# Performance work log

Measured on AMD Instinct MI355X. Metric: run time of the kernel, lower is better.

## Reference

```python
import jax, jax.numpy as jnp
import numpy as np

B, TQ, TY = 8, 400, 400
Q_DIM, Y_DIM, ATT_DIM = 256, 256, 128


def setup_inputs() -> dict:
    key = jax.random.key(0)
    ks = jax.random.split(key, 9)
    s_q = 1.0 / np.sqrt(Q_DIM)
    s_y = 1.0 / np.sqrt(Y_DIM)
    s_a = 1.0 / np.sqrt(ATT_DIM)
    return {
        "query": jax.random.normal(ks[0], (B, TQ, Q_DIM), jnp.float32),
        "y": jax.random.normal(ks[1], (B, TY, Y_DIM), jnp.float32),
        "Wq_w": jax.random.uniform(ks[2], (ATT_DIM, Q_DIM), jnp.float32, -s_q, s_q),
        "Wq_b": jax.random.uniform(ks[3], (ATT_DIM,), jnp.float32, -s_q, s_q),
        "Wy_w": jax.random.uniform(ks[4], (ATT_DIM, Y_DIM), jnp.float32, -s_y, s_y),
        "Wy_b": jax.random.uniform(ks[5], (ATT_DIM,), jnp.float32, -s_y, s_y),
        "v_w": jax.random.uniform(ks[6], (1, ATT_DIM), jnp.float32, -s_a, s_a),
        "v_b": jax.random.uniform(ks[7], (1,), jnp.float32, -s_a, s_a),
        "n_wins_y": jax.random.randint(ks[8], (B,), TY // 2, TY + 1, jnp.int64 if jax.config.jax_enable_x64 else jnp.int32),
    }


def reference(query, y, Wq_w, Wq_b, Wy_w, Wy_b, v_w, v_b, n_wins_y):
    # Bahdanau scores: tanh(Wq(q)[:,None,:,:] + Wy(y)[:,:,None,:]) -> [B,Ty,Tq,A]
    q_proj = jnp.einsum('bqd,ad->bqa', query, Wq_w) + Wq_b      # [B,Tq,A]
    y_proj = jnp.einsum('btd,ad->bta', y, Wy_w) + Wy_b          # [B,Ty,A]
    h = jnp.tanh(q_proj[:, None, :, :] + y_proj[:, :, None, :])  # [B,Ty,Tq,A]
    att = jnp.einsum('btqa,a->btq', h, v_w[0]) + v_b[0]          # [B,Ty,Tq]
    att = jnp.transpose(att, (0, 2, 1))                          # [B,Tq,Ty]
    # mask invalid y windows (dim 2 = Ty), then softmax over Ty
    mask = jnp.arange(att.shape[2])[None, None, :] < n_wins_y[:, None, None]
    att = jnp.where(mask, att, -jnp.inf)
    att = jax.nn.softmax(att, axis=2)
    # soft attention apply: bmm(att, y) -> [B,Tq,y_dim]
    return jnp.einsum('bqt,btd->bqd', att, y)
```

## Files before the change

kernel.cpp:

```cpp
#include <hip/hip_runtime.h>


#define LOG2E 1.4426950408889634f
#define TANH_SCALE 2.8853900817779268f

constexpr int TQn = 400, TYn = 400, AD = 128, DD = 256;
constexpr int QT = 8;
constexpr int QBLOCKS = TQn / QT;
constexpr int YT = 64;
constexpr int NTT = 7;
constexpr int SSTR = 65;
constexpr int AQT = 8;
constexpr int AT3 = 16;
constexpr int PSTR = 449;

__global__ __launch_bounds__(128, 4) void proj_kernel(
    const float* __restrict__ qin, const float* __restrict__ yin,
    const float* __restrict__ Wq, const float* __restrict__ bq,
    const float* __restrict__ Wy, const float* __restrict__ by,
    float* __restrict__ Eq, float* __restrict__ Ey)
{
    const int blk = blockIdx.x;
    const bool is_q = blk < 800;
    const int row0 = (is_q ? blk : blk - 800) * 4;
    const float* in   = (is_q ? qin : yin) + (size_t)row0 * DD;
    const float* W    = is_q ? Wq : Wy;
    const float* bias = is_q ? bq : by;
    float* outp = (is_q ? Eq : Ey) + (size_t)row0 * AD;

    __shared__ float lin[4 * DD];
    {
        const float4* in4 = reinterpret_cast<const float4*>(in);
        float4* l4s = reinterpret_cast<float4*>(lin);
        l4s[threadIdx.x]       = in4[threadIdx.x];
        l4s[threadIdx.x + 128] = in4[threadIdx.x + 128];
    }
    __syncthreads();

    const int a = threadIdx.x;
    float acc0 = 0.f, acc1 = 0.f, acc2 = 0.f, acc3 = 0.f;
    const float4* w4p = reinterpret_cast<const float4*>(W + (size_t)a * DD);
    const float4* l4  = reinterpret_cast<const float4*>(lin);
    #pragma unroll 8
    for (int d4 = 0; d4 < 64; ++d4) {
        float4 w4 = w4p[d4];
        float4 v0 = l4[d4], v1 = l4[64 + d4], v2 = l4[128 + d4], v3 = l4[192 + d4];
        acc0 = fmaf(w4.x, v0.x, acc0); acc0 = fmaf(w4.y, v0.y, acc0);
        acc0 = fmaf(w4.z, v0.z, acc0); acc0 = fmaf(w4.w, v0.w, acc0);
        acc1 = fmaf(w4.x, v1.x, acc1); acc1 = fmaf(w4.y, v1.y, acc1);
        acc1 = fmaf(w4.z, v1.z, acc1); acc1 = fmaf(w4.w, v1.w, acc1);
        acc2 = fmaf(w4.x, v2.x, acc2); acc2 = fmaf(w4.y, v2.y, acc2);
        acc2 = fmaf(w4.z, v2.z, acc2); acc2 = fmaf(w4.w, v2.w, acc2);
        acc3 = fmaf(w4.x, v3.x, acc3); acc3 = fmaf(w4.y, v3.y, acc3);
        acc3 = fmaf(w4.z, v3.z, acc3); acc3 = fmaf(w4.w, v3.w, acc3);
    }
    const float bb = bias[a];
    outp[(size_t)0 * AD + a] = __builtin_amdgcn_exp2f((acc0 + bb) * TANH_SCALE);
    outp[(size_t)1 * AD + a] = __builtin_amdgcn_exp2f((acc1 + bb) * TANH_SCALE);
    outp[(size_t)2 * AD + a] = __builtin_amdgcn_exp2f((acc2 + bb) * TANH_SCALE);
    outp[(size_t)3 * AD + a] = __builtin_amdgcn_exp2f((acc3 + bb) * TANH_SCALE);
}

__global__ __launch_bounds__(512, 2) void score_kernel(
    const float* __restrict__ Eq,
    const float* __restrict__ Ey,
    const float* __restrict__ vw,
    const int*  __restrict__ nwins,
    float* __restrict__ s)
{
    const int bid = blockIdx.x;
    const int b   = bid / (QBLOCKS * NTT);
    const int rem = bid % (QBLOCKS * NTT);
    const int qt  = rem / NTT;
    const int tt  = rem % NTT;
    const int n   = nwins[b];
    const int t0  = tt * YT;
    if (t0 >= n) return;
    const int q0 = qt * QT;

    __shared__ float4 s_eq[QT * 32];
    __shared__ float4 s_v4[32];
    __shared__ float4 s_ey[32 * SSTR];

    const int tid  = threadIdx.x;
    const int wave = tid >> 6;
    const int lane = tid & 63;
    const int pcol = tid & 31;
    const int prow = tid >> 5;

    {
        const float4* eyb = reinterpret_cast<const float4*>(Ey);
        const size_t base = (size_t)(b * TYn) * 32 + pcol;
        const int r1 = min(t0 + prow + 16, TYn - 1);
        const int r2 = min(t0 + prow + 32, TYn - 1);
        const int r3 = min(t0 + prow + 48, TYn - 1);
        s_ey[pcol * SSTR + prow     ] = eyb[base + (size_t)(t0 + prow) * 32];
        s_ey[pcol * SSTR + prow + 16] = eyb[base + (size_t)r1 * 32];
        s_ey[pcol * SSTR + prow + 32] = eyb[base + (size_t)r2 * 32];
        s_ey[pcol * SSTR + prow + 48] = eyb[base + (size_t)r3 * 32];
    }
    if (tid < QT * 32) {
        s_eq[tid] = reinterpret_cast<const float4*>(Eq + (size_t)(b * TQn + q0) * AD)[tid];
    } else if (tid < QT * 32 + 32) {
        float4 v = reinterpret_cast<const float4*>(vw)[tid - QT * 32];
        s_v4[tid - QT * 32] = make_float4(-2.f * v.x, -2.f * v.y, -2.f * v.z, -2.f * v.w);
    }
    __syncthreads();

    float ac0 = 0.f, ac1 = 0.f, ac2 = 0.f, ac3 = 0.f;
    const float4* qrow = s_eq + wave * 32;
    #pragma unroll 8
    for (int a4 = 0; a4 < 32; ++a4) {
        float4 yv = s_ey[a4 * SSTR + lane];
        float4 qv = qrow[a4];
        float4 vv = s_v4[a4];
        float a0 = fmaf(qv.x, yv.x, 1.f);
        float a1 = fmaf(qv.y, yv.y, 1.f);
        float a2 = fmaf(qv.z, yv.z, 1.f);
        float a3 = fmaf(qv.w, yv.w, 1.f);
        float p01 = a0 * a1, p23 = a2 * a3;
        float R = __builtin_amdgcn_rcpf(p01 * p23);
        float u = p23 * R, v = p01 * R;
        ac0 = fmaf(vv.x, a1 * u, ac0);
        ac1 = fmaf(vv.y, a0 * u, ac1);
        ac2 = fmaf(vv.z, a3 * v, ac2);
        ac3 = fmaf(vv.w, a2 * v, ac3);
    }
    const int t = t0 + lane;
    if (t < TYn)
        s[(size_t)(b * TQn + q0 + wave) * TYn + t] = (ac0 + ac1) + (ac2 + ac3);
}

__global__ __launch_bounds__(512, 2) void apply_kernel(
    const float* __restrict__ y,
    const float* __restrict__ s,
    const int*  __restrict__ nwins,
    float* __restrict__ out)
{
    const int bid = blockIdx.x;
    const int b   = bid / QBLOCKS;
    const int q0  = (bid % QBLOCKS) * AQT;
    const int tid = threadIdx.x, wave = tid >> 6, lane = tid & 63;
    const int n = nwins[b];
    const float NEG_INF = -__builtin_inff();

    __shared__ float  s_p[AQT][PSTR];
    __shared__ float4 s_y[2][AT3 * 64];

    const float* srow = s + (size_t)(b * TQn + q0 + wave) * TYn;
    float sc0, sc1, sc2, sc3, sc4, sc5, sc6;
    {
        int t;
        t = 0 * 64 + lane; sc0 = (t < n) ? srow[t] : NEG_INF;
        t = 1 * 64 + lane; sc1 = (t < n) ? srow[t] : NEG_INF;
        t = 2 * 64 + lane; sc2 = (t < n) ? srow[t] : NEG_INF;
        t = 3 * 64 + lane; sc3 = (t < n) ? srow[t] : NEG_INF;
        t = 4 * 64 + lane; sc4 = (t < n) ? srow[t] : NEG_INF;
        t = 5 * 64 + lane; sc5 = (t < n) ? srow[t] : NEG_INF;
        t = 6 * 64 + lane; sc6 = (t < n) ? srow[t] : NEG_INF;
    }
    float m = fmaxf(fmaxf(fmaxf(sc0, sc1), fmaxf(sc2, sc3)),
                    fmaxf(fmaxf(sc4, sc5), sc6));
    #pragma unroll
    for (int off = 32; off >= 1; off >>= 1) m = fmaxf(m, __shfl_xor(m, off, 64));
    sc0 = __builtin_amdgcn_exp2f((sc0 - m) * LOG2E);
    sc1 = __builtin_amdgcn_exp2f((sc1 - m) * LOG2E);
    sc2 = __builtin_amdgcn_exp2f((sc2 - m) * LOG2E);
    sc3 = __builtin_amdgcn_exp2f((sc3 - m) * LOG2E);
    sc4 = __builtin_amdgcn_exp2f((sc4 - m) * LOG2E);
    sc5 = __builtin_amdgcn_exp2f((sc5 - m) * LOG2E);
    sc6 = __builtin_amdgcn_exp2f((sc6 - m) * LOG2E);
    float l = ((sc0 + sc1) + (sc2 + sc3)) + ((sc4 + sc5) + sc6);
    #pragma unroll
    for (int off = 32; off >= 1; off >>= 1) l += __shfl_xor(l, off, 64);
    const float inv = 1.0f / l;
    s_p[wave][0 * 64 + lane] = sc0 * inv;
    s_p[wave][1 * 64 + lane] = sc1 * inv;
    s_p[wave][2 * 64 + lane] = sc2 * inv;
    s_p[wave][3 * 64 + lane] = sc3 * inv;
    s_p[wave][4 * 64 + lane] = sc4 * inv;
    s_p[wave][5 * 64 + lane] = sc5 * inv;
    s_p[wave][6 * 64 + lane] = sc6 * inv;

    const float4* yb = reinterpret_cast<const float4*>(y) + (size_t)(b * TYn) * 64;
    const int scol = tid & 63, srow0 = tid >> 6;
    float4 g0 = yb[(size_t)(srow0    ) * 64 + scol];
    float4 g1 = yb[(size_t)(srow0 + 8) * 64 + scol];

    const int qa = ((wave & 3) << 1) + (lane >> 5);
    const int d4 = ((wave >> 2) << 5) + (lane & 31);
    float4 acc = {0.f, 0.f, 0.f, 0.f};
    const int ntile = (n + AT3 - 1) / AT3;

    __syncthreads();
    for (int i = 0; i < ntile; ++i) {
        float4* buf = s_y[i & 1];
        buf[srow0 * 64 + scol]       = g0;
        buf[(srow0 + 8) * 64 + scol] = g1;
        if (i + 1 < ntile) {
            const int t0n = (i + 1) * AT3;
            g0 = yb[(size_t)(t0n + srow0    ) * 64 + scol];
            g1 = yb[(size_t)(t0n + srow0 + 8) * 64 + scol];
        }
        __syncthreads();
        const int tb = i * AT3;
        #pragma unroll
        for (int ttl = 0; ttl < AT3; ++ttl) {
            float  pt = s_p[qa][tb + ttl];
            float4 yv = buf[ttl * 64 + d4];
            acc.x = fmaf(pt, yv.x, acc.x);
            acc.y = fmaf(pt, yv.y, acc.y);
            acc.z = fmaf(pt, yv.z, acc.z);
            acc.w = fmaf(pt, yv.w, acc.w);
        }
    }
    reinterpret_cast<float4*>(out)[(size_t)(b * TQn + q0 + qa) * 64 + d4] = acc;
}

extern "C" void kernel_launch(void* const* d_in, const int* in_sizes, int n_in,
                              void* d_out, int out_size, void* d_ws, size_t ws_size,
                              hipStream_t stream) {
    const float* query = (const float*)d_in[0];
    const float* y     = (const float*)d_in[1];
    const float* Wq_w  = (const float*)d_in[2];
    const float* Wq_b  = (const float*)d_in[3];
    const float* Wy_w  = (const float*)d_in[4];
    const float* Wy_b  = (const float*)d_in[5];
    const float* v_w   = (const float*)d_in[6];
    const int* nw      = (const int*)d_in[8];
    float* out = (float*)d_out;

    float* Eq = (float*)d_ws;
    float* Ey = Eq + (size_t)8 * TQn * AD;
    float* s  = Ey + (size_t)8 * TYn * AD;

    proj_kernel<<<1600, 128, 0, stream>>>(query, y, Wq_w, Wq_b, Wy_w, Wy_b, Eq, Ey);
    score_kernel<<<8 * QBLOCKS * NTT, 512, 0, stream>>>(Eq, Ey, v_w, nw, s);
    apply_kernel<<<8 * QBLOCKS, 512, 0, stream>>>(y, s, nw, out);
}
```

Measured before the change: 75.30 us.

## Transpose weights, split-K projection, and retile score/apply kernels for 256 threads

Adds a weight transpose kernel so projection loads of W are coalesced across threads, and reworks the projection into 8-row blocks with a two-way split over the reduction dimension plus a shared-memory reduction. The score kernel now computes 4 queries per thread over a quarter of the attention dim and reduces with cross-lane shuffles, which reuses each Ey load across queries. The apply kernel moves to 4 queries per 256-thread block and issues its y prefetch before the softmax. These changes aim at uncoalesced weight reads and low register-level reuse, at the cost of an extra kernel launch and more shuffle and reduction overhead.

```diff
diff --git a/kernel.cpp b/kernel.cpp
--- a/kernel.cpp
+++ b/kernel.cpp
@@ -5,63 +5,76 @@
 #define TANH_SCALE 2.8853900817779268f
 
 constexpr int TQn = 400, TYn = 400, AD = 128, DD = 256;
-constexpr int QT = 8;
-constexpr int QBLOCKS = TQn / QT;
-constexpr int YT = 64;
-constexpr int NTT = 7;
 constexpr int SSTR = 65;
-constexpr int AQT = 8;
-constexpr int AT3 = 16;
-constexpr int PSTR = 449;
-
-__global__ __launch_bounds__(128, 4) void proj_kernel(
+
+__global__ __launch_bounds__(128) void transpose_kernel(
+    const float* __restrict__ Wq, const float* __restrict__ Wy,
+    float4* __restrict__ WTq, float4* __restrict__ WTy)
+{
+    const int k4 = blockIdx.x & 63;
+    const bool isq = blockIdx.x < 64;
+    const float4* src = reinterpret_cast<const float4*>(isq ? Wq : Wy);
+    float4* dst = isq ? WTq : WTy;
+    const int a = threadIdx.x;
+    dst[k4 * 128 + a] = src[a * 64 + k4];
+}
+
+__global__ __launch_bounds__(256, 4) void proj_kernel(
     const float* __restrict__ qin, const float* __restrict__ yin,
-    const float* __restrict__ Wq, const float* __restrict__ bq,
-    const float* __restrict__ Wy, const float* __restrict__ by,
+    const float4* __restrict__ WTq, const float* __restrict__ bq,
+    const float4* __restrict__ WTy, const float* __restrict__ by,
     float* __restrict__ Eq, float* __restrict__ Ey)
 {
     const int blk = blockIdx.x;
-    const bool is_q = blk < 800;
-    const int row0 = (is_q ? blk : blk - 800) * 4;
+    const bool is_q = blk < 400;
+    const int row0 = (is_q ? blk : blk - 400) * 8;
     const float* in   = (is_q ? qin : yin) + (size_t)row0 * DD;
-    const float* W    = is_q ? Wq : Wy;
+    const float4* wt  = is_q ? WTq : WTy;
     const float* bias = is_q ? bq : by;
     float* outp = (is_q ? Eq : Ey) + (size_t)row0 * AD;
 
-    __shared__ float lin[4 * DD];
+    __shared__ float lin[8 * DD];
+    __shared__ float red[8][AD];
     {
         const float4* in4 = reinterpret_cast<const float4*>(in);
         float4* l4s = reinterpret_cast<float4*>(lin);
         l4s[threadIdx.x]       = in4[threadIdx.x];
-        l4s[threadIdx.x + 128] = in4[threadIdx.x + 128];
-    }
-    __syncthreads();
-
-    const int a = threadIdx.x;
-    float acc0 = 0.f, acc1 = 0.f, acc2 = 0.f, acc3 = 0.f;
-    const float4* w4p = reinterpret_cast<const float4*>(W + (size_t)a * DD);
-    const float4* l4  = reinterpret_cast<const float4*>(lin);
+        l4s[threadIdx.x + 256] = in4[threadIdx.x + 256];
+    }
+    __syncthreads();
+
+    const int a = threadIdx.x & 127;
+    const int h = threadIdx.x >> 7;
+    float acc[8] = {0.f,0.f,0.f,0.f,0.f,0.f,0.f,0.f};
+    const float4* l4 = reinterpret_cast<const float4*>(lin);
     #pragma unroll 8
-    for (int d4 = 0; d4 < 64; ++d4) {
-        float4 w4 = w4p[d4];
-        float4 v0 = l4[d4], v1 = l4[64 + d4], v2 = l4[128 + d4], v3 = l4[192 + d4];
-        acc0 = fmaf(w4.x, v0.x, acc0); acc0 = fmaf(w4.y, v0.y, acc0);
-        acc0 = fmaf(w4.z, v0.z, acc0); acc0 = fmaf(w4.w, v0.w, acc0);
-        acc1 = fmaf(w4.x, v1.x, acc1); acc1 = fmaf(w4.y, v1.y, acc1);
-        acc1 = fmaf(w4.z, v1.z, acc1); acc1 = fmaf(w4.w, v1.w, acc1);
-        acc2 = fmaf(w4.x, v2.x, acc2); acc2 = fmaf(w4.y, v2.y, acc2);
-        acc2 = fmaf(w4.z, v2.z, acc2); acc2 = fmaf(w4.w, v2.w, acc2);
-        acc3 = fmaf(w4.x, v3.x, acc3); acc3 = fmaf(w4.y, v3.y, acc3);
-        acc3 = fmaf(w4.z, v3.z, acc3); acc3 = fmaf(w4.w, v3.w, acc3);
-    }
-    const float bb = bias[a];
-    outp[(size_t)0 * AD + a] = __builtin_amdgcn_exp2f((acc0 + bb) * TANH_SCALE);
-    outp[(size_t)1 * AD + a] = __builtin_amdgcn_exp2f((acc1 + bb) * TANH_SCALE);
-    outp[(size_t)2 * AD + a] = __builtin_amdgcn_exp2f((acc2 + bb) * TANH_SCALE);
-    outp[(size_t)3 * AD + a] = __builtin_amdgcn_exp2f((acc3 + bb) * TANH_SCALE);
-}
-
-__global__ __launch_bounds__(512, 2) void score_kernel(
+    for (int i = 0; i < 32; ++i) {
+        const int k4 = h * 32 + i;
+        float4 w4 = wt[k4 * 128 + a];
+        #pragma unroll
+        for (int r = 0; r < 8; ++r) {
+            float4 v = l4[r * 64 + k4];
+            acc[r] = fmaf(w4.x, v.x, acc[r]);
+            acc[r] = fmaf(w4.y, v.y, acc[r]);
+            acc[r] = fmaf(w4.z, v.z, acc[r]);
+            acc[r] = fmaf(w4.w, v.w, acc[r]);
+        }
+    }
+    if (h) {
+        #pragma unroll
+        for (int r = 0; r < 8; ++r) red[r][a] = acc[r];
+    }
+    __syncthreads();
+    if (!h) {
+        const float bb = bias[a];
+        #pragma unroll
+        for (int r = 0; r < 8; ++r)
+            outp[(size_t)r * AD + a] =
+                __builtin_amdgcn_exp2f((acc[r] + red[r][a] + bb) * TANH_SCALE);
+    }
+}
+
+__global__ __launch_bounds__(256, 4) void score_kernel(
     const float* __restrict__ Eq,
     const float* __restrict__ Ey,
     const float* __restrict__ vw,
@@ -69,83 +82,103 @@
     float* __restrict__ s)
 {
     const int bid = blockIdx.x;
-    const int b   = bid / (QBLOCKS * NTT);
-    const int rem = bid % (QBLOCKS * NTT);
-    const int qt  = rem / NTT;
-    const int tt  = rem % NTT;
+    const int b   = bid / 700;
+    const int rem = bid % 700;
+    const int qg  = rem / 7;
+    const int tt  = rem % 7;
     const int n   = nwins[b];
-    const int t0  = tt * YT;
+    const int t0  = tt * 64;
     if (t0 >= n) return;
-    const int q0 = qt * QT;
-
-    __shared__ float4 s_eq[QT * 32];
+    const int q0 = qg * 4;
+
+    __shared__ float4 s_ey[32 * SSTR];
+    __shared__ float4 s_eq4[4 * 32];
     __shared__ float4 s_v4[32];
-    __shared__ float4 s_ey[32 * SSTR];
 
     const int tid  = threadIdx.x;
-    const int wave = tid >> 6;
-    const int lane = tid & 63;
     const int pcol = tid & 31;
     const int prow = tid >> 5;
-
     {
         const float4* eyb = reinterpret_cast<const float4*>(Ey);
         const size_t base = (size_t)(b * TYn) * 32 + pcol;
-        const int r1 = min(t0 + prow + 16, TYn - 1);
-        const int r2 = min(t0 + prow + 32, TYn - 1);
-        const int r3 = min(t0 + prow + 48, TYn - 1);
-        s_ey[pcol * SSTR + prow     ] = eyb[base + (size_t)(t0 + prow) * 32];
-        s_ey[pcol * SSTR + prow + 16] = eyb[base + (size_t)r1 * 32];
-        s_ey[pcol * SSTR + prow + 32] = eyb[base + (size_t)r2 * 32];
-        s_ey[pcol * SSTR + prow + 48] = eyb[base + (size_t)r3 * 32];
-    }
-    if (tid < QT * 32) {
-        s_eq[tid] = reinterpret_cast<const float4*>(Eq + (size_t)(b * TQn + q0) * AD)[tid];
-    } else if (tid < QT * 32 + 32) {
-        float4 v = reinterpret_cast<const float4*>(vw)[tid - QT * 32];
-        s_v4[tid - QT * 32] = make_float4(-2.f * v.x, -2.f * v.y, -2.f * v.z, -2.f * v.w);
-    }
-    __syncthreads();
-
+        #pragma unroll
+        for (int k = 0; k < 8; ++k) {
+            const int rt = min(t0 + prow + 8 * k, TYn - 1);
+            s_ey[pcol * SSTR + prow + 8 * k] = eyb[base + (size_t)rt * 32];
+        }
+    }
+    if (tid < 128) {
+        s_eq4[tid] = reinterpret_cast<const float4*>(Eq + (size_t)(b * TQn + q0) * AD)[tid];
+    } else if (tid < 160) {
+        float4 v = reinterpret_cast<const float4*>(vw)[tid - 128];
+        s_v4[tid - 128] = make_float4(-2.f * v.x, -2.f * v.y, -2.f * v.z, -2.f * v.w);
+    }
+    __syncthreads();
+
+    const int lane = tid & 63;
+    const int wave = tid >> 6;
+    const int tloc = (wave << 4) | (lane & 15);
+    const int ag   = lane >> 4;
     float ac0 = 0.f, ac1 = 0.f, ac2 = 0.f, ac3 = 0.f;
-    const float4* qrow = s_eq + wave * 32;
-    #pragma unroll 8
-    for (int a4 = 0; a4 < 32; ++a4) {
-        float4 yv = s_ey[a4 * SSTR + lane];
-        float4 qv = qrow[a4];
-        float4 vv = s_v4[a4];
-        float a0 = fmaf(qv.x, yv.x, 1.f);
-        float a1 = fmaf(qv.y, yv.y, 1.f);
-        float a2 = fmaf(qv.z, yv.z, 1.f);
-        float a3 = fmaf(qv.w, yv.w, 1.f);
-        float p01 = a0 * a1, p23 = a2 * a3;
-        float R = __builtin_amdgcn_rcpf(p01 * p23);
-        float u = p23 * R, v = p01 * R;
-        ac0 = fmaf(vv.x, a1 * u, ac0);
-        ac1 = fmaf(vv.y, a0 * u, ac1);
-        ac2 = fmaf(vv.z, a3 * v, ac2);
-        ac3 = fmaf(vv.w, a2 * v, ac3);
-    }
-    const int t = t0 + lane;
-    if (t < TYn)
-        s[(size_t)(b * TQn + q0 + wave) * TYn + t] = (ac0 + ac1) + (ac2 + ac3);
-}
-
-__global__ __launch_bounds__(512, 2) void apply_kernel(
+    #pragma unroll
+    for (int i = 0; i < 8; ++i) {
+        const int a4 = ag * 8 + i;
+        const float4 yv = s_ey[a4 * SSTR + tloc];
+        const float4 vv = s_v4[a4];
+        #define SCORE_Q(ACC, QQ)                                            \
+        {                                                                   \
+            float4 qv = s_eq4[(QQ) * 32 + a4];                              \
+            float a0 = fmaf(qv.x, yv.x, 1.f);                               \
+            float a1 = fmaf(qv.y, yv.y, 1.f);                               \
+            float a2 = fmaf(qv.z, yv.z, 1.f);                               \
+            float a3 = fmaf(qv.w, yv.w, 1.f);                               \
+            float p01 = a0 * a1, p23 = a2 * a3;                             \
+            float R = __builtin_amdgcn_rcpf(p01 * p23);                     \
+            float u = p23 * R, w = p01 * R;                                 \
+            ACC = fmaf(vv.x, a1 * u, ACC);                                  \
+            ACC = fmaf(vv.y, a0 * u, ACC);                                  \
+            ACC = fmaf(vv.z, a3 * w, ACC);                                  \
+            ACC = fmaf(vv.w, a2 * w, ACC);                                  \
+        }
+        SCORE_Q(ac0, 0) SCORE_Q(ac1, 1) SCORE_Q(ac2, 2) SCORE_Q(ac3, 3)
+        #undef SCORE_Q
+    }
+    ac0 += __shfl_xor(ac0, 16, 64); ac0 += __shfl_xor(ac0, 32, 64);
+    ac1 += __shfl_xor(ac1, 16, 64); ac1 += __shfl_xor(ac1, 32, 64);
+    ac2 += __shfl_xor(ac2, 16, 64); ac2 += __shfl_xor(ac2, 32, 64);
+    ac3 += __shfl_xor(ac3, 16, 64); ac3 += __shfl_xor(ac3, 32, 64);
+    const int t = t0 + tloc;
+    if (ag == 0 && t < TYn) {
+        const size_t o = (size_t)(b * TQn + q0) * TYn + t;
+        s[o]            = ac0;
+        s[o + TYn]      = ac1;
+        s[o + 2 * TYn]  = ac2;
+        s[o + 3 * TYn]  = ac3;
+    }
+}
+
+__global__ __launch_bounds__(256, 4) void apply_kernel(
     const float* __restrict__ y,
     const float* __restrict__ s,
     const int*  __restrict__ nwins,
     float* __restrict__ out)
 {
     const int bid = blockIdx.x;
-    const int b   = bid / QBLOCKS;
-    const int q0  = (bid % QBLOCKS) * AQT;
+    const int b   = bid / 100;
+    const int q0  = (bid % 100) * 4;
     const int tid = threadIdx.x, wave = tid >> 6, lane = tid & 63;
     const int n = nwins[b];
     const float NEG_INF = -__builtin_inff();
 
-    __shared__ float  s_p[AQT][PSTR];
-    __shared__ float4 s_y[2][AT3 * 64];
+    __shared__ float  s_p[4][408];
+    __shared__ float4 s_y[2][16 * 64];
+
+    const float4* yb = reinterpret_cast<const float4*>(y) + (size_t)(b * TYn) * 64;
+    const int scol = tid & 63, srow0 = tid >> 6;
+    float4 g0 = yb[(size_t)(srow0     ) * 64 + scol];
+    float4 g1 = yb[(size_t)(srow0 +  4) * 64 + scol];
+    float4 g2 = yb[(size_t)(srow0 +  8) * 64 + scol];
+    float4 g3 = yb[(size_t)(srow0 + 12) * 64 + scol];
 
     const float* srow = s + (size_t)(b * TQn + q0 + wave) * TYn;
     float sc0, sc1, sc2, sc3, sc4, sc5, sc6;
@@ -180,41 +213,43 @@
     s_p[wave][3 * 64 + lane] = sc3 * inv;
     s_p[wave][4 * 64 + lane] = sc4 * inv;
     s_p[wave][5 * 64 + lane] = sc5 * inv;
-    s_p[wave][6 * 64 + lane] = sc6 * inv;
-
-    const float4* yb = reinterpret_cast<const float4*>(y) + (size_t)(b * TYn) * 64;
-    const int scol = tid & 63, srow0 = tid >> 6;
-    float4 g0 = yb[(size_t)(srow0    ) * 64 + scol];
-    float4 g1 = yb[(size_t)(srow0 + 8) * 64 + scol];
-
-    const int qa = ((wave & 3) << 1) + (lane >> 5);
-    const int d4 = ((wave >> 2) << 5) + (lane & 31);
+    {
+        const int t = 6 * 64 + lane;
+        if (t < TYn) s_p[wave][t] = sc6 * inv;
+    }
+
+    const int q  = lane >> 4;
+    const int d4 = (wave << 4) | (lane & 15);
     float4 acc = {0.f, 0.f, 0.f, 0.f};
-    const int ntile = (n + AT3 - 1) / AT3;
+    const int ntile = (n + 15) >> 4;
 
     __syncthreads();
     for (int i = 0; i < ntile; ++i) {
         float4* buf = s_y[i & 1];
-        buf[srow0 * 64 + scol]       = g0;
-        buf[(srow0 + 8) * 64 + scol] = g1;
+        buf[(srow0     ) * 64 + scol] = g0;
+        buf[(srow0 +  4) * 64 + scol] = g1;
+        buf[(srow0 +  8) * 64 + scol] = g2;
+        buf[(srow0 + 12) * 64 + scol] = g3;
         if (i + 1 < ntile) {
-            const int t0n = (i + 1) * AT3;
-            g0 = yb[(size_t)(t0n + srow0    ) * 64 + scol];
-            g1 = yb[(size_t)(t0n + srow0 + 8) * 64 + scol];
+            const int t0n = (i + 1) * 16;
+            g0 = yb[(size_t)(t0n + srow0     ) * 64 + scol];
+            g1 = yb[(size_t)(t0n + srow0 +  4) * 64 + scol];
+            g2 = yb[(size_t)(t0n + srow0 +  8) * 64 + scol];
+            g3 = yb[(size_t)(t0n + srow0 + 12) * 64 + scol];
         }
         __syncthreads();
-        const int tb = i * AT3;
-        #pragma unroll
-        for (int ttl = 0; ttl < AT3; ++ttl) {
-            float  pt = s_p[qa][tb + ttl];
-            float4 yv = buf[ttl * 64 + d4];
+        const int tb = i * 16;
+        #pragma unroll
+        for (int ttl = 0; ttl < 16; ++ttl) {
+            const float  pt = s_p[q][tb + ttl];
+            const float4 yv = buf[ttl * 64 + d4];
             acc.x = fmaf(pt, yv.x, acc.x);
             acc.y = fmaf(pt, yv.y, acc.y);
             acc.z = fmaf(pt, yv.z, acc.z);
             acc.w = fmaf(pt, yv.w, acc.w);
         }
     }
-    reinterpret_cast<float4*>(out)[(size_t)(b * TQn + q0 + qa) * 64 + d4] = acc;
+    reinterpret_cast<float4*>(out)[(size_t)(b * TQn + q0 + q) * 64 + d4] = acc;
 }
 
 extern "C" void kernel_launch(void* const* d_in, const int* in_sizes, int n_in,
@@ -230,11 +265,14 @@
     const int* nw      = (const int*)d_in[8];
     float* out = (float*)d_out;
 
-    float* Eq = (float*)d_ws;
-    float* Ey = Eq + (size_t)8 * TQn * AD;
-    float* s  = Ey + (size_t)8 * TYn * AD;
-
-    proj_kernel<<<1600, 128, 0, stream>>>(query, y, Wq_w, Wq_b, Wy_w, Wy_b, Eq, Ey);
-    score_kernel<<<8 * QBLOCKS * NTT, 512, 0, stream>>>(Eq, Ey, v_w, nw, s);
-    apply_kernel<<<8 * QBLOCKS, 512, 0, stream>>>(y, s, nw, out);
-}
+    float4* WTq = (float4*)d_ws;
+    float4* WTy = WTq + 64 * 128;
+    float*  Eq  = (float*)(WTy + 64 * 128);
+    float*  Ey  = Eq + (size_t)8 * TQn * AD;
+    float*  s   = Ey + (size_t)8 * TYn * AD;
+
+    transpose_kernel<<<128, 128, 0, stream>>>(Wq_w, Wy_w, WTq, WTy);
+    proj_kernel<<<800, 256, 0, stream>>>(query, y, WTq, Wq_b, WTy, Wy_b, Eq, Ey);
+    score_kernel<<<8 * 100 * 7, 256, 0, stream>>>(Eq, Ey, v_w, nw, s);
+    apply_kernel<<<8 * 100, 256, 0, stream>>>(y, s, nw, out);
+}
```

Measured after the change: 65.87 us. 1.14x faster.
